# Kernel tuning notes

Hardware: AMD Instinct MI355X
Metric: run time of the kernel (lower is better)

## Reference

```python
import jax, jax.numpy as jnp
import numpy as np


def setup_inputs() -> dict:
    key = jax.random.key(0)
    k1, k2 = jax.random.split(key)
    inputs = jax.random.normal(k1, (16, 64, 64, 512), dtype=jnp.float32)
    gamma = jax.random.uniform(k2, (1,), dtype=jnp.float32)
    return {"inputs": inputs, "gamma": gamma}


def reference(inputs, gamma):
    # inputs: [B, H, W, C] -> vec_a: [B, HW, C]
    B, H, W, C = inputs.shape
    vec_a = inputs.reshape(B, H * W, C)
    # channel gram matrix: [B, C, C]
    aTa = jnp.einsum('bnc,bnd->bcd', vec_a, vec_a)
    # softmax over last axis (Keras Activation('softmax') default)
    attn = jax.nn.softmax(aTa, axis=-1)
    # attn @ a^T: [B, C, HW] -> transpose -> [B, HW, C]
    aaTa = jnp.einsum('bcd,bnd->bnc', attn, vec_a)
    out = gamma * aaTa.reshape(B, H, W, C) + inputs
    return out
```

## Files before the change

kernel.cpp:

```cpp
#include <hip/hip_runtime.h>

#define BATCH 16
#define NHW 4096
#define CH 512
#define SPLITK 2

typedef __attribute__((ext_vector_type(8))) short bf16x8;
typedef __attribute__((ext_vector_type(4))) float f32x4;

__device__ __forceinline__ short f2bf(float f) {
  union { float f; unsigned u; } c; c.f = f;
  unsigned u = c.u;
  unsigned r = (u + 0x7FFFu + ((u >> 16) & 1u)) >> 16;
  return (short)r;
}

__device__ __forceinline__ void gload_lds16(const void* g, void* l) {
  __builtin_amdgcn_global_load_lds((const __attribute__((address_space(1))) unsigned*)g,
                                   (__attribute__((address_space(3))) unsigned*)l,
                                   16, 0, 0);
}

__device__ __forceinline__ void stage32(const short* __restrict__ g, int ld, int rowbase, int kk,
                                        short* lbase, int w, int l) {
#pragma unroll
  for (int i = 0; i < 4; ++i) {
    const int row = w * 32 + i * 8 + (l >> 3);
    const short* gs = g + (size_t)(rowbase + row) * ld + kk + (l & 7) * 8;
    short* ls = lbase + (w * 32 + i * 8) * 64;
    gload_lds16(gs, ls);
  }
}

__device__ __forceinline__ void gemm_body(const short* __restrict__ Ag, int lda,
                                          const short* __restrict__ Bg, int ldb,
                                          int m0, int n0, int kbase, int nkt,
                                          short* lds, f32x4 acc[4][4]) {
  const int tid = threadIdx.x;
  const int l = tid & 63;
  const int w = tid >> 6;
  const int wr = w >> 1;
  const int wc = w & 1;

#pragma unroll
  for (int mi = 0; mi < 4; ++mi)
#pragma unroll
    for (int ni = 0; ni < 4; ++ni)
      acc[mi][ni] = (f32x4){0.f, 0.f, 0.f, 0.f};

  stage32(Ag, lda, m0, kbase, lds, w, l);
  stage32(Bg, ldb, n0, kbase, lds + 8192, w, l);
  __syncthreads();

  int cur = 0;
  for (int t = 0; t < nkt; ++t) {
    if (t + 1 < nkt) {
      short* nb = lds + (cur ^ 1) * 16384;
      stage32(Ag, lda, m0, kbase + (t + 1) * 64, nb, w, l);
      stage32(Bg, ldb, n0, kbase + (t + 1) * 64, nb + 8192, w, l);
    }
    const short* As = lds + cur * 16384;
    const short* Bs = As + 8192;
#pragma unroll
    for (int ks = 0; ks < 2; ++ks) {
      const int ko = ks * 32 + (l >> 4) * 8;
      bf16x8 af[4], bfv[4];
#pragma unroll
      for (int mi = 0; mi < 4; ++mi)
        af[mi] = *(const bf16x8*)(As + (wr * 64 + mi * 16 + (l & 15)) * 64 + ko);
#pragma unroll
      for (int ni = 0; ni < 4; ++ni)
        bfv[ni] = *(const bf16x8*)(Bs + (wc * 64 + ni * 16 + (l & 15)) * 64 + ko);
#pragma unroll
      for (int mi = 0; mi < 4; ++mi)
#pragma unroll
        for (int ni = 0; ni < 4; ++ni)
          acc[mi][ni] = __builtin_amdgcn_mfma_f32_16x16x32_bf16(af[mi], bfv[ni], acc[mi][ni], 0, 0, 0);
    }
    __syncthreads();
    cur ^= 1;
  }
}

__global__ __launch_bounds__(256) void cast_transpose(const float* __restrict__ in,
                                                      short* __restrict__ A16,
                                                      short* __restrict__ At16) {
  __shared__ float tile[32][33];
  const int b = blockIdx.z;
  const int n0 = blockIdx.x * 32;
  const int c0 = blockIdx.y * 32;
  const int tx = threadIdx.x, ty = threadIdx.y;
  const float* src = in + ((size_t)b * NHW + n0) * CH + c0;
#pragma unroll
  for (int i = 0; i < 4; ++i) {
    const int r = ty + i * 8;
    const float v = src[(size_t)r * CH + tx];
    tile[r][tx] = v;
    A16[((size_t)b * NHW + n0 + r) * CH + c0 + tx] = f2bf(v);
  }
  __syncthreads();
#pragma unroll
  for (int i = 0; i < 4; ++i) {
    const int cr = ty + i * 8;
    At16[((size_t)b * CH + c0 + cr) * NHW + n0 + tx] = f2bf(tile[tx][cr]);
  }
}

__global__ __launch_bounds__(256) void gram_kernel(const short* __restrict__ At,
                                                   float* __restrict__ Gp) {
  __shared__ short lds[32768];
  const int b = blockIdx.z;
  const int m0 = (blockIdx.x >> 2) * 128;
  const int n0 = (blockIdx.x & 3) * 128;
  const int kbase = blockIdx.y * (NHW / SPLITK);
  const short* Ab = At + (size_t)b * CH * NHW;
  f32x4 acc[4][4];
  gemm_body(Ab, NHW, Ab, NHW, m0, n0, kbase, (NHW / SPLITK) / 64, lds, acc);

  const int l = threadIdx.x & 63;
  const int w = threadIdx.x >> 6;
  const int wr = w >> 1, wc = w & 1;
  float* G = Gp + (size_t)(blockIdx.y * BATCH + b) * CH * CH;
#pragma unroll
  for (int mi = 0; mi < 4; ++mi)
#pragma unroll
    for (int ni = 0; ni < 4; ++ni) {
      const int col = n0 + wc * 64 + ni * 16 + (l & 15);
      const int rbase = m0 + wr * 64 + mi * 16 + (l >> 4) * 4;
#pragma unroll
      for (int j = 0; j < 4; ++j)
        G[(size_t)(rbase + j) * CH + col] = acc[mi][ni][j];
    }
}

__global__ __launch_bounds__(64) void softmax_kernel(const float* __restrict__ Gp,
                                                     short* __restrict__ P) {
  const int row = blockIdx.x;
  const int b = row >> 9;
  const int c = row & 511;
  const int l = threadIdx.x;
  const float* g0 = Gp + ((size_t)b * CH + c) * CH;
  const float* g1 = Gp + ((size_t)(BATCH + b) * CH + c) * CH;
  float v[8];
#pragma unroll
  for (int i = 0; i < 8; ++i) v[i] = g0[l + i * 64] + g1[l + i * 64];
  float m = v[0];
#pragma unroll
  for (int i = 1; i < 8; ++i) m = fmaxf(m, v[i]);
  for (int off = 32; off > 0; off >>= 1) m = fmaxf(m, __shfl_xor(m, off, 64));
  float s = 0.f;
#pragma unroll
  for (int i = 0; i < 8; ++i) { v[i] = __expf(v[i] - m); s += v[i]; }
  for (int off = 32; off > 0; off >>= 1) s += __shfl_xor(s, off, 64);
  const float inv = 1.0f / s;
  short* p = P + ((size_t)b * CH + c) * CH;
#pragma unroll
  for (int i = 0; i < 8; ++i) p[l + i * 64] = f2bf(v[i] * inv);
}

__global__ __launch_bounds__(256) void out_kernel(const short* __restrict__ A16,
                                                  const short* __restrict__ P,
                                                  const float* __restrict__ inp,
                                                  const float* __restrict__ gamma,
                                                  float* __restrict__ out) {
  __shared__ short lds[32768];
  const int b = blockIdx.z;
  const int m0 = (blockIdx.x >> 2) * 128;
  const int n0 = (blockIdx.x & 3) * 128;
  const short* Ab = A16 + (size_t)b * NHW * CH;
  const short* Pb = P + (size_t)b * CH * CH;
  f32x4 acc[4][4];
  gemm_body(Ab, CH, Pb, CH, m0, n0, 0, CH / 64, lds, acc);

  const float gm = gamma[0];
  const int l = threadIdx.x & 63;
  const int w = threadIdx.x >> 6;
  const int wr = w >> 1, wc = w & 1;
  const float* ib = inp + (size_t)b * NHW * CH;
  float* ob = out + (size_t)b * NHW * CH;
#pragma unroll
  for (int mi = 0; mi < 4; ++mi)
#pragma unroll
    for (int ni = 0; ni < 4; ++ni) {
      const int col = n0 + wc * 64 + ni * 16 + (l & 15);
      const int rbase = m0 + wr * 64 + mi * 16 + (l >> 4) * 4;
#pragma unroll
      for (int j = 0; j < 4; ++j) {
        const size_t idx = (size_t)(rbase + j) * CH + col;
        ob[idx] = gm * acc[mi][ni][j] + ib[idx];
      }
    }
}

extern "C" void kernel_launch(void* const* d_in, const int* in_sizes, int n_in,
                              void* d_out, int out_size, void* d_ws, size_t ws_size,
                              hipStream_t stream) {
  const float* inp = (const float*)d_in[0];
  const float* gamma = (const float*)d_in[1];
  float* out = (float*)d_out;
  char* ws = (char*)d_ws;
  short* A16 = (short*)ws;
  short* At16 = (short*)(ws + (size_t)67108864);
  float* Gp = (float*)(ws + (size_t)134217728);
  short* P = (short*)(ws + (size_t)167772160);

  hipLaunchKernelGGL(cast_transpose, dim3(NHW / 32, CH / 32, BATCH), dim3(32, 8), 0, stream,
                     inp, A16, At16);
  hipLaunchKernelGGL(gram_kernel, dim3(16, SPLITK, BATCH), dim3(256), 0, stream, At16, Gp);
  hipLaunchKernelGGL(softmax_kernel, dim3(BATCH * CH), dim3(64), 0, stream, Gp, P);
  hipLaunchKernelGGL(out_kernel, dim3((NHW / 128) * (CH / 128), 1, BATCH), dim3(256), 0, stream,
                     A16, P, inp, gamma, out);
}
```

Before: 383.2 us.

## Vectorize cast-transpose, remap blocks across XCDs, read P directly from global

```diff
diff --git a/kernel.cpp b/kernel.cpp
--- a/kernel.cpp
+++ b/kernel.cpp
@@ -6,6 +6,7 @@
 #define SPLITK 2
 
 typedef __attribute__((ext_vector_type(8))) short bf16x8;
+typedef __attribute__((ext_vector_type(4))) short s16x4;
 typedef __attribute__((ext_vector_type(4))) float f32x4;
 
 __device__ __forceinline__ short f2bf(float f) {
@@ -32,32 +33,75 @@
   }
 }
 
-__device__ __forceinline__ void gemm_body(const short* __restrict__ Ag, int lda,
-                                          const short* __restrict__ Bg, int ldb,
-                                          int m0, int n0, int kbase, int nkt,
-                                          short* lds, f32x4 acc[4][4]) {
+__global__ __launch_bounds__(256) void cast_transpose(const float* __restrict__ in,
+                                                      short* __restrict__ A16,
+                                                      short* __restrict__ At16) {
+  __shared__ short t[64][66];
+  const int b = blockIdx.z;
+  const int n0 = blockIdx.x * 64;
+  const int c0 = blockIdx.y * 64;
+  const int tid = threadIdx.x;
+  const int rr = tid >> 4;
+  const int cq = (tid & 15) * 4;
+  const float* src = in + ((size_t)b * NHW + n0) * CH + c0;
+  short* a = A16 + ((size_t)b * NHW + n0) * CH + c0;
+#pragma unroll
+  for (int i = 0; i < 4; ++i) {
+    const int r = rr + i * 16;
+    const float4 v = *(const float4*)(src + (size_t)r * CH + cq);
+    s16x4 s;
+    s.x = f2bf(v.x); s.y = f2bf(v.y); s.z = f2bf(v.z); s.w = f2bf(v.w);
+    *(s16x4*)(a + (size_t)r * CH + cq) = s;
+    t[cq + 0][r] = s.x; t[cq + 1][r] = s.y; t[cq + 2][r] = s.z; t[cq + 3][r] = s.w;
+  }
+  __syncthreads();
+  short* at = At16 + ((size_t)b * CH + c0) * NHW + n0;
+#pragma unroll
+  for (int i = 0; i < 4; ++i) {
+    const int c = rr + i * 16;
+    s16x4 s;
+    s.x = t[c][cq]; s.y = t[c][cq + 1]; s.z = t[c][cq + 2]; s.w = t[c][cq + 3];
+    *(s16x4*)(at + (size_t)c * NHW + cq) = s;
+  }
+}
+
+__global__ __launch_bounds__(256) void gram_kernel(const short* __restrict__ At,
+                                                   float* __restrict__ Gp) {
+  __shared__ short lds[32768];
+  const int flat = blockIdx.x;
+  const int wg = (flat & 7) * 64 + (flat >> 3);
+  const int b = wg >> 5;
+  const int r5 = wg & 31;
+  const int kchunk = r5 >> 4;
+  const int tile = r5 & 15;
+  const int m0 = (tile >> 2) * 128;
+  const int n0 = (tile & 3) * 128;
+  const int kbase = kchunk * (NHW / SPLITK);
+
   const int tid = threadIdx.x;
   const int l = tid & 63;
   const int w = tid >> 6;
-  const int wr = w >> 1;
-  const int wc = w & 1;
-
+  const int wr = w >> 1, wc = w & 1;
+  const short* Ab = At + (size_t)b * CH * NHW;
+
+  f32x4 acc[4][4];
 #pragma unroll
   for (int mi = 0; mi < 4; ++mi)
 #pragma unroll
     for (int ni = 0; ni < 4; ++ni)
       acc[mi][ni] = (f32x4){0.f, 0.f, 0.f, 0.f};
 
-  stage32(Ag, lda, m0, kbase, lds, w, l);
-  stage32(Bg, ldb, n0, kbase, lds + 8192, w, l);
+  stage32(Ab, NHW, m0, kbase, lds, w, l);
+  stage32(Ab, NHW, n0, kbase, lds + 8192, w, l);
   __syncthreads();
 
+  const int nkt = (NHW / SPLITK) / 64;
   int cur = 0;
   for (int t = 0; t < nkt; ++t) {
     if (t + 1 < nkt) {
       short* nb = lds + (cur ^ 1) * 16384;
-      stage32(Ag, lda, m0, kbase + (t + 1) * 64, nb, w, l);
-      stage32(Bg, ldb, n0, kbase + (t + 1) * 64, nb + 8192, w, l);
+      stage32(Ab, NHW, m0, kbase + (t + 1) * 64, nb, w, l);
+      stage32(Ab, NHW, n0, kbase + (t + 1) * 64, nb + 8192, w, l);
     }
     const short* As = lds + cur * 16384;
     const short* Bs = As + 8192;
@@ -80,47 +124,8 @@
     __syncthreads();
     cur ^= 1;
   }
-}
-
-__global__ __launch_bounds__(256) void cast_transpose(const float* __restrict__ in,
-                                                      short* __restrict__ A16,
-                                                      short* __restrict__ At16) {
-  __shared__ float tile[32][33];
-  const int b = blockIdx.z;
-  const int n0 = blockIdx.x * 32;
-  const int c0 = blockIdx.y * 32;
-  const int tx = threadIdx.x, ty = threadIdx.y;
-  const float* src = in + ((size_t)b * NHW + n0) * CH + c0;
-#pragma unroll
-  for (int i = 0; i < 4; ++i) {
-    const int r = ty + i * 8;
-    const float v = src[(size_t)r * CH + tx];
-    tile[r][tx] = v;
-    A16[((size_t)b * NHW + n0 + r) * CH + c0 + tx] = f2bf(v);
-  }
-  __syncthreads();
-#pragma unroll
-  for (int i = 0; i < 4; ++i) {
-    const int cr = ty + i * 8;
-    At16[((size_t)b * CH + c0 + cr) * NHW + n0 + tx] = f2bf(tile[tx][cr]);
-  }
-}
-
-__global__ __launch_bounds__(256) void gram_kernel(const short* __restrict__ At,
-                                                   float* __restrict__ Gp) {
-  __shared__ short lds[32768];
-  const int b = blockIdx.z;
-  const int m0 = (blockIdx.x >> 2) * 128;
-  const int n0 = (blockIdx.x & 3) * 128;
-  const int kbase = blockIdx.y * (NHW / SPLITK);
-  const short* Ab = At + (size_t)b * CH * NHW;
-  f32x4 acc[4][4];
-  gemm_body(Ab, NHW, Ab, NHW, m0, n0, kbase, (NHW / SPLITK) / 64, lds, acc);
-
-  const int l = threadIdx.x & 63;
-  const int w = threadIdx.x >> 6;
-  const int wr = w >> 1, wc = w & 1;
-  float* G = Gp + (size_t)(blockIdx.y * BATCH + b) * CH * CH;
+
+  float* G = Gp + (size_t)(kchunk * BATCH + b) * CH * CH;
 #pragma unroll
   for (int mi = 0; mi < 4; ++mi)
 #pragma unroll
@@ -163,19 +168,58 @@
                                                   const float* __restrict__ inp,
                                                   const float* __restrict__ gamma,
                                                   float* __restrict__ out) {
-  __shared__ short lds[32768];
-  const int b = blockIdx.z;
-  const int m0 = (blockIdx.x >> 2) * 128;
-  const int n0 = (blockIdx.x & 3) * 128;
+  __shared__ short lds[16384];
+  const int flat = blockIdx.x;
+  const int wg = (flat & 7) * 256 + (flat >> 3);
+  const int b = wg >> 7;
+  const int t7 = wg & 127;
+  const int m0 = (t7 >> 2) * 128;
+  const int n0 = (t7 & 3) * 128;
+
+  const int tid = threadIdx.x;
+  const int l = tid & 63;
+  const int w = tid >> 6;
+  const int wr = w >> 1, wc = w & 1;
   const short* Ab = A16 + (size_t)b * NHW * CH;
   const short* Pb = P + (size_t)b * CH * CH;
+
   f32x4 acc[4][4];
-  gemm_body(Ab, CH, Pb, CH, m0, n0, 0, CH / 64, lds, acc);
+#pragma unroll
+  for (int mi = 0; mi < 4; ++mi)
+#pragma unroll
+    for (int ni = 0; ni < 4; ++ni)
+      acc[mi][ni] = (f32x4){0.f, 0.f, 0.f, 0.f};
+
+  stage32(Ab, CH, m0, 0, lds, w, l);
+  __syncthreads();
+
+  int cur = 0;
+#pragma unroll 1
+  for (int kt = 0; kt < CH / 64; ++kt) {
+    if (kt + 1 < CH / 64)
+      stage32(Ab, CH, m0, (kt + 1) * 64, lds + (cur ^ 1) * 8192, w, l);
+    const short* As = lds + cur * 8192;
+#pragma unroll
+    for (int ks = 0; ks < 2; ++ks) {
+      const int ko = kt * 64 + ks * 32 + (l >> 4) * 8;
+      bf16x8 af[4], bfv[4];
+#pragma unroll
+      for (int ni = 0; ni < 4; ++ni)
+        bfv[ni] = *(const bf16x8*)(Pb + (size_t)(n0 + wc * 64 + ni * 16 + (l & 15)) * CH + ko);
+#pragma unroll
+      for (int mi = 0; mi < 4; ++mi)
+        af[mi] = *(const bf16x8*)(As + (wr * 64 + mi * 16 + (l & 15)) * 64 + ks * 32 + (l >> 4) * 8);
+#pragma unroll
+      for (int mi = 0; mi < 4; ++mi)
+#pragma unroll
+        for (int ni = 0; ni < 4; ++ni)
+          acc[mi][ni] = __builtin_amdgcn_mfma_f32_16x16x32_bf16(af[mi], bfv[ni], acc[mi][ni], 0, 0, 0);
+    }
+    __syncthreads();
+    cur ^= 1;
+  }
 
   const float gm = gamma[0];
-  const int l = threadIdx.x & 63;
-  const int w = threadIdx.x >> 6;
-  const int wr = w >> 1, wc = w & 1;
   const float* ib = inp + (size_t)b * NHW * CH;
   float* ob = out + (size_t)b * NHW * CH;
 #pragma unroll
@@ -204,10 +248,10 @@
   float* Gp = (float*)(ws + (size_t)134217728);
   short* P = (short*)(ws + (size_t)167772160);
 
-  hipLaunchKernelGGL(cast_transpose, dim3(NHW / 32, CH / 32, BATCH), dim3(32, 8), 0, stream,
+  hipLaunchKernelGGL(cast_transpose, dim3(NHW / 64, CH / 64, BATCH), dim3(256), 0, stream,
                      inp, A16, At16);
-  hipLaunchKernelGGL(gram_kernel, dim3(16, SPLITK, BATCH), dim3(256), 0, stream, At16, Gp);
+  hipLaunchKernelGGL(gram_kernel, dim3(16 * SPLITK * BATCH), dim3(256), 0, stream, At16, Gp);
   hipLaunchKernelGGL(softmax_kernel, dim3(BATCH * CH), dim3(64), 0, stream, Gp, P);
-  hipLaunchKernelGGL(out_kernel, dim3((NHW / 128) * (CH / 128), 1, BATCH), dim3(256), 0, stream,
+  hipLaunchKernelGGL(out_kernel, dim3((NHW / 128) * (CH / 128) * BATCH), dim3(256), 0, stream,
                      A16, P, inp, gamma, out);
 }
```

Result: slower. 394.8 us (+3.0%).
